# Optimization experiments

Hardware: AMD Instinct MI355X
Metric: run time of the kernel (lower is better)

## Reference

```python
import jax, jax.numpy as jnp
import numpy as np
from jax import lax

V, E, H = 32000, 256, 512
B, S_SRC, S_TGT = 32, 128, 64


def setup_inputs() -> dict:
    key = jax.random.key(0)
    ks = jax.random.split(key, 16)
    n = lambda k, shp: jax.random.normal(k, shp, dtype=jnp.float32) * 0.05
    return {
        "src": jax.random.randint(ks[0], (B, S_SRC), 0, V, dtype=jnp.int32),
        "tgt": jax.random.randint(ks[1], (B, S_TGT), 0, V, dtype=jnp.int32),
        "enc_emb": n(ks[2], (V, E)),
        "enc_Wih": n(ks[3], (4 * H, E)),
        "enc_Whh": n(ks[4], (4 * H, H)),
        "enc_b": n(ks[5], (4 * H,)),
        "attn_W": n(ks[6], (H, 2 * H)),
        "attn_b": n(ks[7], (H,)),
        "attn_v": jax.random.uniform(ks[8], (H,), dtype=jnp.float32),
        "dec_emb": n(ks[9], (V, E)),
        "dec_Wih": n(ks[10], (4 * H, E + H)),
        "dec_Whh": n(ks[11], (4 * H, H)),
        "dec_b": n(ks[12], (4 * H,)),
        "out_W": n(ks[13], (V, H)),
        "out_b": n(ks[14], (V,)),
    }


def _lstm_cell(x, h, c, Wih, Whh, b):
    # PyTorch gate order: i, f, g, o. b = b_ih + b_hh fused.
    z = x @ Wih.T + h @ Whh.T + b  # [B, 4H]
    i, f, g, o = jnp.split(z, 4, axis=-1)
    c_new = jax.nn.sigmoid(f) * c + jax.nn.sigmoid(i) * jnp.tanh(g)
    h_new = jax.nn.sigmoid(o) * jnp.tanh(c_new)
    return h_new, c_new


def reference(src, tgt, enc_emb, enc_Wih, enc_Whh, enc_b, attn_W, attn_b,
              attn_v, dec_emb, dec_Wih, dec_Whh, dec_b, out_W, out_b):
    b = src.shape[0]
    h0 = jnp.zeros((b, H), dtype=enc_emb.dtype)
    c0 = jnp.zeros((b, H), dtype=enc_emb.dtype)

    # ---- Encoder: single-layer LSTM over src ----
    emb_src = enc_emb[src]  # [B, S_src, E]

    def enc_step(carry, x_t):
        h, c = carry
        h, c = _lstm_cell(x_t, h, c, enc_Wih, enc_Whh, enc_b)
        return (h, c), h

    (h, c), enc_out = lax.scan(enc_step, (h0, c0), emb_src.transpose(1, 0, 2))
    enc_out = enc_out.transpose(1, 0, 2)  # [B, S_src, H]

    # attn_W acts on cat([hidden, enc]); split into hidden and encoder parts.
    W_h = attn_W[:, :H]   # [H, H]
    W_e = attn_W[:, H:]   # [H, H]
    enc_proj = jnp.einsum('bsh,kh->bsk', enc_out, W_e)  # precomputed [B, S, H]

    # ---- Decoder with per-step Bahdanau attention ----
    emb_tgt = dec_emb[tgt].transpose(1, 0, 2)  # [T, B, E]

    def dec_step(carry, e_t):
        h, c = carry
        energy = jnp.tanh(enc_proj + (h @ W_h.T + attn_b)[:, None, :])  # [B,S,H]
        score = energy @ attn_v                                          # [B,S]
        a = jax.nn.softmax(score, axis=1)
        context = jnp.einsum('bs,bsh->bh', a, enc_out)                   # [B,H]
        x = jnp.concatenate([e_t, context], axis=-1)                     # [B,E+H]
        h, c = _lstm_cell(x, h, c, dec_Wih, dec_Whh, dec_b)
        return (h, c), h

    _, dec_h = lax.scan(dec_step, (h, c), emb_tgt)
    dec_h = dec_h.transpose(1, 0, 2)  # [B, T, H]

    return dec_h @ out_W.T + out_b  # [B, T, V]
```

## Files before the change

### kernel.cpp

```cpp
#include <hip/hip_runtime.h>

#define B_    32
#define SSRC  128
#define STGT  64
#define E_    256
#define H_    512
#define G4    2048
#define V_    32000

typedef unsigned short u16;
typedef short bf16x8 __attribute__((ext_vector_type(8)));
typedef float f32x4 __attribute__((ext_vector_type(4)));

__device__ __forceinline__ u16 f2b(float f) {
  unsigned u = __float_as_uint(f);
  u += 0x7FFFu + ((u >> 16) & 1u);
  return (u16)(u >> 16);
}
__device__ __forceinline__ float b2f(u16 h) {
  return __uint_as_float(((unsigned)h) << 16);
}
__device__ __forceinline__ unsigned pk2(float lo, float hi) {
  return (unsigned)f2b(lo) | (((unsigned)f2b(hi)) << 16);
}
__device__ __forceinline__ float sigm(float x) { return 1.0f / (1.0f + __expf(-x)); }
__device__ __forceinline__ float tanh_(float x) { return 1.0f - 2.0f / (1.0f + __expf(2.0f * x)); }

#if defined(__has_builtin)
#if __has_builtin(__builtin_amdgcn_fdot2_f32_bf16)
#define HAS_DOT2 1
#endif
#endif
#ifdef HAS_DOT2
typedef __bf16 b162 __attribute__((ext_vector_type(2)));
__device__ __forceinline__ float dot2u(unsigned a, unsigned b, float acc) {
  return __builtin_amdgcn_fdot2_f32_bf16(__builtin_bit_cast(b162, a),
                                         __builtin_bit_cast(b162, b), acc, false);
}
#else
__device__ __forceinline__ float dot2u(unsigned a, unsigned b, float acc) {
  acc += __uint_as_float(a << 16) * __uint_as_float(b << 16);
  acc += __uint_as_float(a & 0xffff0000u) * __uint_as_float(b & 0xffff0000u);
  return acc;
}
#endif
__device__ __forceinline__ float dot4(uint4 w, uint4 h, float acc) {
  return dot2u(w.w, h.w, dot2u(w.z, h.z, dot2u(w.y, h.y, dot2u(w.x, h.x, acc))));
}

__device__ __forceinline__ int swz64(int c) {
  return (c & ~3) | ((c & 3) ^ ((c >> 3) & 3));
}

__device__ __forceinline__ uint4 cload4(const void* p) {
  uint4 r;
  asm volatile("global_load_dwordx4 %0, %1, off sc0 sc1\n\ts_waitcnt vmcnt(0)"
               : "=&v"(r) : "v"(p) : "memory");
  return r;
}
__device__ __forceinline__ void cstoref(float* p, float v) {
  asm volatile("global_store_dword %0, %1, off sc0 sc1" :: "v"(p), "v"(v) : "memory");
}
__device__ __forceinline__ void cstoreu(unsigned* p, unsigned v) {
  asm volatile("global_store_dword %0, %1, off sc0 sc1" :: "v"(p), "v"(v) : "memory");
}
__device__ __forceinline__ float cloadf_relaxed(const float* p) {
  return __hip_atomic_load(p, __ATOMIC_RELAXED, __HIP_MEMORY_SCOPE_AGENT);
}

__device__ __forceinline__ void arrive(int* flags, int myid, int target) {
  asm volatile("s_waitcnt vmcnt(0)" ::: "memory");
  __syncthreads();
  if (threadIdx.x == 0)
    __hip_atomic_store(flags + myid, target, __ATOMIC_RELAXED, __HIP_MEMORY_SCOPE_AGENT);
}
__device__ __forceinline__ void waitbar(int* flags, int target) {
  if (threadIdx.x < 64) {
    int l = threadIdx.x & 31;
    while (__hip_atomic_load(flags + l, __ATOMIC_RELAXED, __HIP_MEMORY_SCOPE_AGENT) < target)
      __builtin_amdgcn_s_sleep(1);
  }
  __syncthreads();
  asm volatile("" ::: "memory");
}
__device__ __forceinline__ void gbar(int* flags, int myid, int target) {
  arrive(flags, myid, target);
  waitbar(flags, target);
}

__global__ void prep_kernel(const int* __restrict__ src, const int* __restrict__ tgt,
                            const float* __restrict__ enc_emb, const float* __restrict__ dec_emb,
                            const float* __restrict__ enc_Wih, const float* __restrict__ dec_Wih,
                            const float* __restrict__ attn_W, const float* __restrict__ out_W,
                            u16* __restrict__ A_enc, u16* __restrict__ A_dec,
                            u16* __restrict__ WihE, u16* __restrict__ WihD,
                            u16* __restrict__ Web, u16* __restrict__ WihCp,
                            u16* __restrict__ outWb)
{
  const long n_outw = (long)V_ * H_;
  const long n_aenc = (long)B_ * SSRC * E_;
  const long n_adec = (long)B_ * STGT * E_;
  const long n_wih  = (long)G4 * E_;
  const long n_web  = (long)H_ * H_;
  const long n_wcp  = (long)G4 * H_;
  const long total = n_outw + n_aenc + n_adec + 2 * n_wih + n_web + n_wcp;
  for (long i = (long)blockIdx.x * blockDim.x + threadIdx.x; i < total;
       i += (long)gridDim.x * blockDim.x) {
    long x = i;
    if (x < n_outw) { outWb[x] = f2b(out_W[x]); continue; }
    x -= n_outw;
    if (x < n_aenc) {
      int row = (int)(x >> 8), e = (int)(x & 255);
      A_enc[x] = f2b(enc_emb[(size_t)src[row] * E_ + e]);
      continue;
    }
    x -= n_aenc;
    if (x < n_adec) {
      int row = (int)(x >> 8), e = (int)(x & 255);
      A_dec[x] = f2b(dec_emb[(size_t)tgt[row] * E_ + e]);
      continue;
    }
    x -= n_adec;
    if (x < n_wih) { WihE[x] = f2b(enc_Wih[x]); continue; }
    x -= n_wih;
    if (x < n_wih) {
      int r = (int)(x >> 8), e = (int)(x & 255);
      WihD[x] = f2b(dec_Wih[(size_t)r * 768 + e]);
      continue;
    }
    x -= n_wih;
    if (x < n_web) {
      int d = (int)(x >> 9), k = (int)(x & 511);
      Web[x] = f2b(attn_W[(size_t)d * 1024 + 512 + k]);
      continue;
    }
    x -= n_web;
    {
      int n = (int)(x >> 9), k = (int)(x & 511);
      int gb = n >> 6, gate = (n >> 4) & 3, jl = n & 15;
      int orig = gate * 512 + gb * 16 + jl;
      WihCp[x] = f2b(dec_Wih[(size_t)orig * 768 + 256 + k]);
    }
  }
}

template<int KTOT, bool OBF>
__global__ __launch_bounds__(256, 2) void gemm_nt(
    const u16* __restrict__ A, const u16* __restrict__ Bm,
    const float* __restrict__ bias, void* __restrict__ Cv, int M, int N)
{
  int nbm = M >> 7;
  int bn = blockIdx.x / nbm;
  int bm = blockIdx.x % nbm;
  int w = threadIdx.x >> 6, l = threadIdx.x & 63;
  int wr = w >> 1, wc = w & 1;
  int m0 = bm * 128 + wr * 64, n0 = bn * 128 + wc * 64;
  int lr = l & 15, ko = (l >> 4) * 8;
  f32x4 acc[4][4] = {};
  const u16* Ap = A + (size_t)(m0 + lr) * KTOT + ko;
  const u16* Bp = Bm + (size_t)(n0 + lr) * KTOT + ko;
  for (int k0 = 0; k0 < KTOT; k0 += 32) {
    bf16x8 af[4], bfr[4];
#pragma unroll
    for (int i = 0; i < 4; ++i) af[i] = *(const bf16x8*)(Ap + (size_t)i * 16 * KTOT + k0);
#pragma unroll
    for (int i = 0; i < 4; ++i) bfr[i] = *(const bf16x8*)(Bp + (size_t)i * 16 * KTOT + k0);
#pragma unroll
    for (int i = 0; i < 4; ++i)
#pragma unroll
      for (int j = 0; j < 4; ++j)
        acc[i][j] = __builtin_amdgcn_mfma_f32_16x16x32_bf16(af[i], bfr[j], acc[i][j], 0, 0, 0);
  }
  int rbase = (l >> 4) * 4;
#pragma unroll
  for (int i = 0; i < 4; ++i) {
#pragma unroll
    for (int j = 0; j < 4; ++j) {
      int gn = n0 + j * 16 + lr;
      float bv = bias ? bias[gn] : 0.f;
#pragma unroll
      for (int r = 0; r < 4; ++r) {
        int gm = m0 + i * 16 + rbase + r;
        float v = acc[i][j][r] + bv;
        if (OBF) ((u16*)Cv)[(size_t)gm * N + gn] = f2b(v);
        else     ((float*)Cv)[(size_t)gm * N + gn] = v;
      }
    }
  }
}

__device__ __forceinline__ void zgemv64(int tid, const uint4* Wu, const uint4* Hu,
                                        float (*part)[64][4]) {
  int rq = tid >> 4, kq = tid & 15;
  float acc[4][4] = {};
#pragma unroll
  for (int u = 0; u < 4; ++u) {
    int sc = swz64(kq * 4 + u);
    uint4 h0 = Hu[sc], h1 = Hu[64 + sc], h2 = Hu[128 + sc], h3 = Hu[192 + sc];
#pragma unroll
    for (int r = 0; r < 4; ++r) {
      uint4 wv = Wu[(rq * 4 + r) * 64 + sc];
      acc[r][0] = dot4(wv, h0, acc[r][0]);
      acc[r][1] = dot4(wv, h1, acc[r][1]);
      acc[r][2] = dot4(wv, h2, acc[r][2]);
      acc[r][3] = dot4(wv, h3, acc[r][3]);
    }
  }
#pragma unroll
  for (int r = 0; r < 4; ++r) {
    float4 v = {acc[r][0], acc[r][1], acc[r][2], acc[r][3]};
    *(float4*)&part[kq][(rq * 4 + r) ^ (kq & 7)][0] = v;
  }
}

template<typename GrowF>
__device__ __forceinline__ void fillw64(int tid, const float* Wsrc, uint4* Wu, GrowF grow) {
#pragma unroll 4
  for (int i = 0; i < 16; ++i) {
    int idx4 = tid + i * 256;
    int row = idx4 >> 6, c = idx4 & 63;
    const float* s = Wsrc + (size_t)grow(row) * 512 + c * 8;
    float4 a = *(const float4*)s, b4 = *(const float4*)(s + 4);
    uint4 pkv = {pk2(a.x, a.y), pk2(a.z, a.w), pk2(b4.x, b4.y), pk2(b4.z, b4.w)};
    Wu[row * 64 + swz64(c)] = pkv;
  }
}

__global__ __launch_bounds__(256, 1) void encoder_kernel(
    const float* __restrict__ enc_Whh, const u16* __restrict__ encXW,
    unsigned* __restrict__ h16buf ,
    float* __restrict__ cfin, u16* __restrict__ eo_g, int* __restrict__ bars)
{
  const int tid = threadIdx.x;
  const int g = blockIdx.x & 7;
  const int gb = blockIdx.x >> 3;
  const int b0 = g * 4;
  const int ds0 = gb * 16;
  int* flags = bars + g * 64;

  __shared__ uint4 encW4[64 * 64];
  __shared__ uint4 hl16[4 * 64];
  __shared__ float part[16][64][4];
  __shared__ float zx[4][64];
  __shared__ float cS[4][16];

  if (tid < 64) cS[tid >> 4][tid & 15] = 0.f;
  fillw64(tid, enc_Whh, encW4, [&](int row) { return (row >> 4) * 512 + ds0 + (row & 15); });
  __syncthreads();

  const int bl_c = tid >> 6, rl_c = tid & 63;
  const int grow_c = (rl_c >> 4) * 512 + ds0 + (rl_c & 15);
  const u16* xwp = encXW + (size_t)(b0 + bl_c) * SSRC * G4 + grow_c;

  for (int t = 0; t < SSRC; ++t) {
    u16 xw = xwp[(size_t)t * G4];
    {
      int row = tid >> 6, c = tid & 63;
      uint4 v = cload4((const uint4*)h16buf + (size_t)(t & 1) * 2048 + (b0 + row) * 64 + c);
      hl16[row * 64 + swz64(c)] = v;
    }
    __syncthreads();
    zgemv64(tid, encW4, hl16, part);
    __syncthreads();
    {
      float z = 0.f;
#pragma unroll
      for (int kq = 0; kq < 16; ++kq) z += part[kq][rl_c ^ (kq & 7)][bl_c];
      z += b2f(xw);
      zx[bl_c][rl_c] = z;
    }
    __syncthreads();
    if (tid < 64) {
      int bl = tid >> 4, jl = tid & 15;
      float iv = zx[bl][jl], fv = zx[bl][16 + jl], gv = zx[bl][32 + jl], ov = zx[bl][48 + jl];
      float cn = sigm(fv) * cS[bl][jl] + sigm(iv) * tanh_(gv);
      float hn = sigm(ov) * tanh_(cn);
      cS[bl][jl] = cn;
      eo_g[((size_t)(b0 + bl) * SSRC + t) * H_ + ds0 + jl] = f2b(hn);
      float hn1 = __shfl_down(hn, 1);
      if ((jl & 1) == 0)
        cstoreu(h16buf + (size_t)((t + 1) & 1) * 8192 + (size_t)(b0 + bl) * 256 + gb * 8 + (jl >> 1),
                pk2(hn, hn1));
    }
    gbar(flags, gb, t + 1);
  }
  if (tid < 64)
    cfin[(size_t)(b0 + (tid >> 4)) * H_ + ds0 + (tid & 15)] = cS[tid >> 4][tid & 15];
}

__global__ __launch_bounds__(256, 1) void decoder_kernel(
    const float* __restrict__ dec_Whh, const float* __restrict__ attn_W,
    const float* __restrict__ attn_b, const float* __restrict__ attn_v,
    const u16* __restrict__ eprojb, const u16* __restrict__ decXW,
    const u16* __restrict__ eoPb,
    unsigned* __restrict__ hd16, const float* __restrict__ cfin,
    float* __restrict__ vpart ,
    u16* __restrict__ dech, int* __restrict__ bars)
{
  const int tid = threadIdx.x;
  const int g = blockIdx.x & 7;
  const int gb = blockIdx.x >> 3;
  const int b0 = g * 4;
  const int ds0 = gb * 16;
  int* flags = bars + g * 64;
  int ep_ = 0;

  __shared__ uint4 decW4[64 * 64];
  __shared__ uint4 Whb4[16 * 64];
  __shared__ uint4 epL[512][2];
  __shared__ uint4 hl16[4 * 64];
  __shared__ float part[16][64][4];
  __shared__ float partE[8][64][4];
  __shared__ float scoreS[4][128];
  __shared__ float aS[4][128];
  __shared__ float zx[4][64];
  __shared__ float qS[4][16];
  __shared__ float cS[4][16];
  __shared__ float vS[16], bS[16];

  if (tid < 64) cS[tid >> 4][tid & 15] = cfin[(size_t)(b0 + (tid >> 4)) * H_ + ds0 + (tid & 15)];
  if (tid < 16) { vS[tid] = attn_v[ds0 + tid]; bS[tid] = attn_b[ds0 + tid]; }
  fillw64(tid, dec_Whh, decW4, [&](int row) { return (row >> 4) * 512 + ds0 + (row & 15); });
#pragma unroll
  for (int i = 0; i < 4; ++i) {
    int idx4 = tid + i * 256;
    int row = idx4 >> 6, c = idx4 & 63;
    const float* s = attn_W + (size_t)(ds0 + row) * 1024 + c * 8;
    float4 a = *(const float4*)s, b4 = *(const float4*)(s + 4);
    uint4 pkv = {pk2(a.x, a.y), pk2(a.z, a.w), pk2(b4.x, b4.y), pk2(b4.z, b4.w)};
    Whb4[row * 64 + (c ^ (row & 7))] = pkv;
  }
#pragma unroll
  for (int r = 0; r < 2; ++r) {
    int idx = tid + r * 256;
    int b_l = idx >> 7, s = idx & 127;
    const uint4* ep = (const uint4*)(eprojb + (((size_t)(b0 + b_l) * SSRC + s) << 9) + ds0);
    epL[idx][0] = ep[0];
    epL[idx][1] = ep[1];
  }
  const int sq = tid >> 5, cp = tid & 31;
  const int n32 = gb * 32 + cp;
  uint4 eor[16];
  {
    const unsigned* eoPu = (const unsigned*)eoPb;
#pragma unroll
    for (int si = 0; si < 16; ++si) {
      int s = sq * 16 + si;
      eor[si].x = eoPu[((size_t)(b0 + 0) * SSRC + s) * 1024 + n32];
      eor[si].y = eoPu[((size_t)(b0 + 1) * SSRC + s) * 1024 + n32];
      eor[si].z = eoPu[((size_t)(b0 + 2) * SSRC + s) * 1024 + n32];
      eor[si].w = eoPu[((size_t)(b0 + 3) * SSRC + s) * 1024 + n32];
    }
  }
  __syncthreads();

  const int bl_c = tid >> 6, rl_c = tid & 63;
  const int grow_c = (rl_c >> 4) * 512 + ds0 + (rl_c & 15);
  const u16* xwp = decXW + (size_t)(b0 + bl_c) * STGT * G4 + grow_c;

  for (int t = 0; t < STGT; ++t) {
    u16 xw = xwp[(size_t)t * G4];
    {
      int row = tid >> 6, c = tid & 63;
      uint4 v = cload4((const uint4*)hd16 + (b0 + row) * 64 + c);
      hl16[row * 64 + swz64(c)] = v;
    }
    __syncthreads();
    {
      int b_l = tid >> 6, d_l = (tid >> 2) & 15, kq4 = tid & 3;
      float acc = 0.f;
#pragma unroll
      for (int u = 0; u < 16; ++u) {
        int c = kq4 * 16 + u;
        acc = dot4(Whb4[d_l * 64 + (c ^ (d_l & 7))], hl16[b_l * 64 + swz64(c)], acc);
      }
      acc += __shfl_xor(acc, 1);
      acc += __shfl_xor(acc, 2);
      if (kq4 == 0) qS[b_l][d_l] = acc + bS[d_l];
    }
    __syncthreads();
    {
      float* vp = vpart + ((size_t)g * 32 + gb) * 512;
#pragma unroll
      for (int r = 0; r < 2; ++r) {
        int idx = tid + r * 256;
        int b_l = idx >> 7;
        uint4 e0 = epL[idx][0], e1 = epL[idx][1];
        float acc = 0.f;
        acc += vS[0]  * tanh_(b2f((u16)(e0.x & 0xffff)) + qS[b_l][0]);
        acc += vS[1]  * tanh_(b2f((u16)(e0.x >> 16))    + qS[b_l][1]);
        acc += vS[2]  * tanh_(b2f((u16)(e0.y & 0xffff)) + qS[b_l][2]);
        acc += vS[3]  * tanh_(b2f((u16)(e0.y >> 16))    + qS[b_l][3]);
        acc += vS[4]  * tanh_(b2f((u16)(e0.z & 0xffff)) + qS[b_l][4]);
        acc += vS[5]  * tanh_(b2f((u16)(e0.z >> 16))    + qS[b_l][5]);
        acc += vS[6]  * tanh_(b2f((u16)(e0.w & 0xffff)) + qS[b_l][6]);
        acc += vS[7]  * tanh_(b2f((u16)(e0.w >> 16))    + qS[b_l][7]);
        acc += vS[8]  * tanh_(b2f((u16)(e1.x & 0xffff)) + qS[b_l][8]);
        acc += vS[9]  * tanh_(b2f((u16)(e1.x >> 16))    + qS[b_l][9]);
        acc += vS[10] * tanh_(b2f((u16)(e1.y & 0xffff)) + qS[b_l][10]);
        acc += vS[11] * tanh_(b2f((u16)(e1.y >> 16))    + qS[b_l][11]);
        acc += vS[12] * tanh_(b2f((u16)(e1.z & 0xffff)) + qS[b_l][12]);
        acc += vS[13] * tanh_(b2f((u16)(e1.z >> 16))    + qS[b_l][13]);
        acc += vS[14] * tanh_(b2f((u16)(e1.w & 0xffff)) + qS[b_l][14]);
        acc += vS[15] * tanh_(b2f((u16)(e1.w >> 16))    + qS[b_l][15]);
        cstoref(vp + idx, acc);
      }
    }
    arrive(flags, gb, ++ep_);
    zgemv64(tid, decW4, hl16, part);
    waitbar(flags, ep_);

    {
      int b_l = tid >> 6, s0 = (tid & 63) * 2;
      float a0 = 0.f, a1 = 0.f;
#pragma unroll 8
      for (int j = 0; j < 32; ++j) {
        const float* p = vpart + ((size_t)g * 32 + j) * 512 + b_l * 128 + s0;
        a0 += cloadf_relaxed(p);
        a1 += cloadf_relaxed(p + 1);
      }
      scoreS[b_l][s0] = a0;
      scoreS[b_l][s0 + 1] = a1;
    }
    __syncthreads();
    {
      int w = tid >> 6, lane = tid & 63;
      float s1 = scoreS[w][lane], s2v = scoreS[w][64 + lane];
      float m = fmaxf(s1, s2v);
#pragma unroll
      for (int off = 32; off; off >>= 1) m = fmaxf(m, __shfl_xor(m, off));
      float e1 = __expf(s1 - m), e2 = __expf(s2v - m);
      float sm = e1 + e2;
#pragma unroll
      for (int off = 32; off; off >>= 1) sm += __shfl_xor(sm, off);
      float inv = 1.0f / sm;
      aS[w][lane] = e1 * inv;
      aS[w][64 + lane] = e2 * inv;
    }
    __syncthreads();
    {
      float a0 = 0.f, a1 = 0.f, a2 = 0.f, a3 = 0.f, a4 = 0.f, a5 = 0.f, a6 = 0.f, a7 = 0.f;
#pragma unroll
      for (int si = 0; si < 16; ++si) {
        int s = sq * 16 + si;
        float w0 = aS[0][s], w1 = aS[1][s], w2 = aS[2][s], w3 = aS[3][s];
        unsigned u0 = eor[si].x, u1 = eor[si].y, u2 = eor[si].z, u3 = eor[si].w;
        a0 += w0 * b2f((u16)(u0 & 0xffff)); a1 += w0 * b2f((u16)(u0 >> 16));
        a2 += w1 * b2f((u16)(u1 & 0xffff)); a3 += w1 * b2f((u16)(u1 >> 16));
        a4 += w2 * b2f((u16)(u2 & 0xffff)); a5 += w2 * b2f((u16)(u2 >> 16));
        a6 += w3 * b2f((u16)(u3 & 0xffff)); a7 += w3 * b2f((u16)(u3 >> 16));
      }
      int r0 = cp * 2;
      float4 lo = {a0, a2, a4, a6}, hi = {a1, a3, a5, a7};
      *(float4*)&partE[sq][r0][0] = lo;
      *(float4*)&partE[sq][r0 + 1][0] = hi;
    }
    __syncthreads();
    {
      float z = 0.f;
#pragma unroll
      for (int kq = 0; kq < 16; ++kq) z += part[kq][rl_c ^ (kq & 7)][bl_c];
#pragma unroll
      for (int sq2 = 0; sq2 < 8; ++sq2) z += partE[sq2][rl_c][bl_c];
      z += b2f(xw);
      zx[bl_c][rl_c] = z;
    }
    __syncthreads();
    if (tid < 64) {
      int bl = tid >> 4, jl = tid & 15;
      float iv = zx[bl][jl], fv = zx[bl][16 + jl], gv = zx[bl][32 + jl], ov = zx[bl][48 + jl];
      float cn = sigm(fv) * cS[bl][jl] + sigm(iv) * tanh_(gv);
      float hn = sigm(ov) * tanh_(cn);
      cS[bl][jl] = cn;
      dech[((size_t)(b0 + bl) * STGT + t) * H_ + ds0 + jl] = f2b(hn);
      float hn1 = __shfl_down(hn, 1);
      if ((jl & 1) == 0)
        cstoreu(hd16 + (size_t)(b0 + bl) * 256 + gb * 8 + (jl >> 1), pk2(hn, hn1));
    }
    arrive(flags, gb, ++ep_);
    waitbar(flags, ep_);
  }
}

#define OFF_BARE   0u
#define OFF_BARD   2048u
#define OFF_H16    4096u
#define OFF_CFIN   69632u
#define OFF_VPART  135168u
#define OFF_AENC   659456u
#define OFF_ADEC   2756608u
#define OFF_WIHE   3805184u
#define OFF_WIHD   4853760u
#define OFF_WEB    5902336u
#define OFF_WIHCP  6426624u
#define OFF_OUTW   8523776u
#define OFF_ENCXW  41291776u
#define OFF_DECXW  58068992u
#define OFF_EO     66457600u
#define OFF_EPROJ  70651904u
#define OFF_DECH   74846208u

extern "C" void kernel_launch(void* const* d_in, const int* in_sizes, int n_in,
                              void* d_out, int out_size, void* d_ws, size_t ws_size,
                              hipStream_t stream)
{
  const int*   src     = (const int*)d_in[0];
  const int*   tgt     = (const int*)d_in[1];
  const float* enc_emb = (const float*)d_in[2];
  const float* enc_Wih = (const float*)d_in[3];
  const float* enc_Whh = (const float*)d_in[4];
  const float* enc_b   = (const float*)d_in[5];
  const float* attn_W  = (const float*)d_in[6];
  const float* attn_b  = (const float*)d_in[7];
  const float* attn_v  = (const float*)d_in[8];
  const float* dec_emb = (const float*)d_in[9];
  const float* dec_Wih = (const float*)d_in[10];
  const float* dec_Whh = (const float*)d_in[11];
  const float* dec_b   = (const float*)d_in[12];
  const float* out_W   = (const float*)d_in[13];
  const float* out_b   = (const float*)d_in[14];

  char* ws = (char*)d_ws;
  int*      barE   = (int*)(ws + OFF_BARE);
  int*      barD   = (int*)(ws + OFF_BARD);
  unsigned* h16buf = (unsigned*)(ws + OFF_H16);
  float*    cfin   = (float*)(ws + OFF_CFIN);
  float*    vpart  = (float*)(ws + OFF_VPART);
  u16*      A_enc  = (u16*)(ws + OFF_AENC);
  u16*      A_dec  = (u16*)(ws + OFF_ADEC);
  u16*      WihE   = (u16*)(ws + OFF_WIHE);
  u16*      WihD   = (u16*)(ws + OFF_WIHD);
  u16*      Web    = (u16*)(ws + OFF_WEB);
  u16*      WihCp  = (u16*)(ws + OFF_WIHCP);
  u16*      outWb  = (u16*)(ws + OFF_OUTW);
  u16*      encXW  = (u16*)(ws + OFF_ENCXW);
  u16*      eoPb   = (u16*)(ws + OFF_ENCXW);
  u16*      decXW  = (u16*)(ws + OFF_DECXW);
  u16*      eo_g   = (u16*)(ws + OFF_EO);
  u16*      eprojb = (u16*)(ws + OFF_EPROJ);
  u16*      dech   = (u16*)(ws + OFF_DECH);

  (void)hipMemsetAsync(d_ws, 0, OFF_H16 + 65536, stream);

  prep_kernel<<<2048, 256, 0, stream>>>(src, tgt, enc_emb, dec_emb, enc_Wih, dec_Wih,
                                        attn_W, out_W, A_enc, A_dec, WihE, WihD, Web, WihCp, outWb);

  gemm_nt<256, true><<<512, 256, 0, stream>>>(A_enc, WihE, enc_b, (void*)encXW, 4096, 2048);
  gemm_nt<256, true><<<256, 256, 0, stream>>>(A_dec, WihD, dec_b, (void*)decXW, 2048, 2048);

  encoder_kernel<<<256, 256, 0, stream>>>(enc_Whh, encXW, h16buf, cfin, eo_g, barE);

  gemm_nt<512, true><<<128, 256, 0, stream>>>(eo_g, Web, nullptr, (void*)eprojb, 4096, 512);
  gemm_nt<512, true><<<512, 256, 0, stream>>>(eo_g, WihCp, nullptr, (void*)eoPb, 4096, 2048);

  decoder_kernel<<<256, 256, 0, stream>>>(dec_Whh, attn_W, attn_b, attn_v,
                                          eprojb, decXW, eoPb, h16buf, cfin,
                                          vpart, dech, barD);

  gemm_nt<512, false><<<4000, 256, 0, stream>>>(dech, outWb, out_b, d_out, 2048, 32000);
}
```

Baseline: 1.388 ms.

## Fuse barrier wait with hidden-state load and prefetch next-step input in recurrent loops

The grid-barrier wait now runs inside the same 64 threads that load the fresh hidden state. They issue cache-bypassing loads into shared memory right after the flag poll, which removes one __syncthreads and a separate global load phase from each recurrent step. The next step's input-projection value is prefetched between arrive and wait, and the barrier after the final step is skipped. The GEMM block index is also remapped across the 8-way block interleave, apparently to spread tiles across XCDs. The risks are that 64 threads each issue 4 loads serially, and that the inline asm cache-control flags must be correct for coherence.

Measured after the change: 1.407 ms. Within noise of the previous version (+1.4%).

```diff
diff --git a/kernel.cpp b/kernel.cpp
--- a/kernel.cpp
+++ b/kernel.cpp
@@ -83,9 +83,35 @@
   __syncthreads();
   asm volatile("" ::: "memory");
 }
-__device__ __forceinline__ void gbar(int* flags, int myid, int target) {
-  arrive(flags, myid, target);
-  waitbar(flags, target);
+
+__device__ __forceinline__ void waitload_h(int* flags, int target,
+                                           const unsigned* hd, int b0, uint4* hl16) {
+  const int tid = threadIdx.x;
+  if (tid < 64) {
+    int l = tid & 31;
+    while (__hip_atomic_load(flags + l, __ATOMIC_RELAXED, __HIP_MEMORY_SCOPE_AGENT) < target)
+      __builtin_amdgcn_s_sleep(1);
+    const uint4* src = (const uint4*)hd + (size_t)b0 * 64;
+    int row = tid >> 4;
+    int c0 = (tid & 15) * 4;
+    const uint4* p0 = src + row * 64 + c0;
+    uint4 a, b, c, d;
+    asm volatile(
+        "global_load_dwordx4 %0, %4, off sc0 sc1\n\t"
+        "global_load_dwordx4 %1, %5, off sc0 sc1\n\t"
+        "global_load_dwordx4 %2, %6, off sc0 sc1\n\t"
+        "global_load_dwordx4 %3, %7, off sc0 sc1\n\t"
+        "s_waitcnt vmcnt(0)"
+        : "=&v"(a), "=&v"(b), "=&v"(c), "=&v"(d)
+        : "v"(p0), "v"(p0 + 1), "v"(p0 + 2), "v"(p0 + 3)
+        : "memory");
+    hl16[row * 64 + swz64(c0 + 0)] = a;
+    hl16[row * 64 + swz64(c0 + 1)] = b;
+    hl16[row * 64 + swz64(c0 + 2)] = c;
+    hl16[row * 64 + swz64(c0 + 3)] = d;
+  }
+  __syncthreads();
+  asm volatile("" ::: "memory");
 }
 
 __global__ void prep_kernel(const int* __restrict__ src, const int* __restrict__ tgt,
@@ -149,9 +175,10 @@
     const u16* __restrict__ A, const u16* __restrict__ Bm,
     const float* __restrict__ bias, void* __restrict__ Cv, int M, int N)
 {
+  int nid = ((blockIdx.x & 7) * (gridDim.x >> 3)) + (blockIdx.x >> 3);
   int nbm = M >> 7;
-  int bn = blockIdx.x / nbm;
-  int bm = blockIdx.x % nbm;
+  int bn = nid / nbm;
+  int bm = nid % nbm;
   int w = threadIdx.x >> 6, l = threadIdx.x & 63;
   int wr = w >> 1, wc = w & 1;
   int m0 = bm * 128 + wr * 64, n0 = bn * 128 + wc * 64;
@@ -246,20 +273,20 @@
 
   if (tid < 64) cS[tid >> 4][tid & 15] = 0.f;
   fillw64(tid, enc_Whh, encW4, [&](int row) { return (row >> 4) * 512 + ds0 + (row & 15); });
-  __syncthreads();
 
   const int bl_c = tid >> 6, rl_c = tid & 63;
   const int grow_c = (rl_c >> 4) * 512 + ds0 + (rl_c & 15);
   const u16* xwp = encXW + (size_t)(b0 + bl_c) * SSRC * G4 + grow_c;
 
+  {
+    int row = tid >> 6, c = tid & 63;
+    uint4 v = cload4((const uint4*)h16buf + (b0 + row) * 64 + c);
+    hl16[row * 64 + swz64(c)] = v;
+  }
+  u16 xw = xwp[0];
+  __syncthreads();
+
   for (int t = 0; t < SSRC; ++t) {
-    u16 xw = xwp[(size_t)t * G4];
-    {
-      int row = tid >> 6, c = tid & 63;
-      uint4 v = cload4((const uint4*)h16buf + (size_t)(t & 1) * 2048 + (b0 + row) * 64 + c);
-      hl16[row * 64 + swz64(c)] = v;
-    }
-    __syncthreads();
     zgemv64(tid, encW4, hl16, part);
     __syncthreads();
     {
@@ -282,7 +309,11 @@
         cstoreu(h16buf + (size_t)((t + 1) & 1) * 8192 + (size_t)(b0 + bl) * 256 + gb * 8 + (jl >> 1),
                 pk2(hn, hn1));
     }
-    gbar(flags, gb, t + 1);
+    if (t < SSRC - 1) {
+      arrive(flags, gb, t + 1);
+      xw = xwp[(size_t)(t + 1) * G4];
+      waitload_h(flags, t + 1, h16buf + (size_t)((t + 1) & 1) * 8192, b0, hl16);
+    }
   }
   if (tid < 64)
     cfin[(size_t)(b0 + (tid >> 4)) * H_ + ds0 + (tid & 15)] = cS[tid >> 4][tid & 15];
@@ -352,20 +383,20 @@
       eor[si].w = eoPu[((size_t)(b0 + 3) * SSRC + s) * 1024 + n32];
     }
   }
-  __syncthreads();
 
   const int bl_c = tid >> 6, rl_c = tid & 63;
   const int grow_c = (rl_c >> 4) * 512 + ds0 + (rl_c & 15);
   const u16* xwp = decXW + (size_t)(b0 + bl_c) * STGT * G4 + grow_c;
 
+  {
+    int row = tid >> 6, c = tid & 63;
+    uint4 v = cload4((const uint4*)hd16 + (b0 + row) * 64 + c);
+    hl16[row * 64 + swz64(c)] = v;
+  }
+  u16 xw = xwp[0];
+  __syncthreads();
+
   for (int t = 0; t < STGT; ++t) {
-    u16 xw = xwp[(size_t)t * G4];
-    {
-      int row = tid >> 6, c = tid & 63;
-      uint4 v = cload4((const uint4*)hd16 + (b0 + row) * 64 + c);
-      hl16[row * 64 + swz64(c)] = v;
-    }
-    __syncthreads();
     {
       int b_l = tid >> 6, d_l = (tid >> 2) & 15, kq4 = tid & 3;
       float acc = 0.f;
@@ -477,8 +508,11 @@
       if ((jl & 1) == 0)
         cstoreu(hd16 + (size_t)(b0 + bl) * 256 + gb * 8 + (jl >> 1), pk2(hn, hn1));
     }
-    arrive(flags, gb, ++ep_);
-    waitbar(flags, ep_);
+    if (t < STGT - 1) {
+      arrive(flags, gb, ++ep_);
+      xw = xwp[(size_t)(t + 1) * G4];
+      waitload_h(flags, ep_, hd16, b0, hl16);
+    }
   }
 }
 
```
